# Performance work log

Measured on AMD Instinct MI355X. Metric: run time of the kernel, lower is better.

## Reference

```python
import jax, jax.numpy as jnp
import numpy as np

V, E, CIN, COUT, NH, HID = 8192, 2048, 128, 128, 4, 32
EPS = 1e-5

def _ln(x, g, b):
    m = x.mean(-1, keepdims=True)
    v = x.var(-1, keepdims=True)
    return (x - m) / jnp.sqrt(v + EPS) * g + b

def setup_inputs() -> dict:
    key = jax.random.key(0)
    ks = jax.random.split(key, 12)
    s = 0.05
    X = jax.random.normal(ks[0], (V, CIN), jnp.float32)
    H = jax.random.bernoulli(ks[1], 0.02, (V, E)).astype(jnp.float32)
    edge_features = jax.random.normal(ks[2], (E, COUT), jnp.float32)
    Wv = jax.random.normal(ks[3], (CIN, COUT), jnp.float32) * s
    bv = jnp.zeros((COUT,), jnp.float32)
    We = jax.random.normal(ks[4], (COUT, COUT), jnp.float32) * s
    be = jnp.zeros((COUT,), jnp.float32)
    vW1 = jax.random.normal(ks[5], (NH, CIN, HID), jnp.float32) * s
    vb1 = jnp.zeros((NH, HID), jnp.float32)
    vW2 = jax.random.normal(ks[6], (NH, HID), jnp.float32) * s
    vb2 = jnp.zeros((NH,), jnp.float32)
    eW1 = jax.random.normal(ks[7], (COUT, HID), jnp.float32) * s
    eb1 = jnp.zeros((HID,), jnp.float32)
    eW2 = jax.random.normal(ks[8], (HID,), jnp.float32) * s
    eb2 = jnp.zeros((), jnp.float32)
    Wc = jax.random.normal(ks[9], (NH * COUT, COUT), jnp.float32) * s
    bc = jnp.zeros((COUT,), jnp.float32)
    Wg = jax.random.normal(ks[10], (CIN + COUT, COUT), jnp.float32) * s
    bg = jnp.zeros((COUT,), jnp.float32)
    return dict(X=X, H=H, edge_features=edge_features, Wv=Wv, bv=bv, We=We, be=be,
                vW1=vW1, vb1=vb1, vW2=vW2, vb2=vb2, eW1=eW1, eb1=eb1, eW2=eW2, eb2=eb2,
                Wc=Wc, bc=bc,
                ln_e_g=jnp.ones((COUT,), jnp.float32), ln_e_b=jnp.zeros((COUT,), jnp.float32),
                ln_v_g=jnp.ones((COUT,), jnp.float32), ln_v_b=jnp.zeros((COUT,), jnp.float32),
                bn_g=jnp.ones((COUT,), jnp.float32), bn_b=jnp.zeros((COUT,), jnp.float32),
                Wg=Wg, bg=bg)

def reference(X, H, edge_features, Wv, bv, We, be, vW1, vb1, vW2, vb2,
              eW1, eb1, eW2, eb2, Wc, bc, ln_e_g, ln_e_b, ln_v_g, ln_v_b,
              bn_g, bn_b, Wg, bg):
    gelu = lambda t: jax.nn.gelu(t, approximate=False)  # torch nn.GELU default (erf)
    Ht = H.T                                   # (E, V)
    Xt = X @ Wv + bv                           # (V, Cout) theta_v
    # per-head vertex attention MLP: Linear(Cin,32)->GELU->Linear(32,1), vectorized over heads
    hid = gelu(jnp.einsum('vc,hck->hvk', X, vW1) + vb1[:, None, :])
    attn = jax.nn.sigmoid(jnp.einsum('hvk,hk->hv', hid, vW2) + vb2[:, None])  # (NH, V)
    deg = Ht.sum(axis=1, keepdims=True)        # (E, 1) edge degrees
    denom = jnp.maximum(deg, 1.0)
    # degree-normalized attention-weighted v2e aggregation per head
    head_e = jnp.einsum('ev,hvc->hec', Ht, Xt[None] * attn[:, :, None]) / denom[None]
    e_cat = jnp.transpose(head_e, (1, 0, 2)).reshape(E, NH * COUT)  # concat heads dim=1
    e_feat = e_cat @ Wc + bc                   # attn_combine
    # edge attention uses the LAST head's vertex weights (global-var quirk in torch code)
    edge_att = ((Ht @ attn[-1]) / jnp.maximum(deg[:, 0], 1.0))[:, None]  # (E,1)
    # edge-feature gating with e_attention head 0
    te = edge_features @ We + be               # theta_e
    e_scores = gelu(e_feat @ eW1 + eb1) @ eW2 + eb2
    ew = jax.nn.sigmoid(e_scores)[:, None]
    e_feat = e_feat * ew + te * (1.0 - ew)
    # normalize == 'both': layer_norm_e then batch_norm (training-mode batch stats)
    e_feat = _ln(e_feat, ln_e_g, ln_e_b)
    m = e_feat.mean(axis=0)
    v = e_feat.var(axis=0)
    e_feat = (e_feat - m) / jnp.sqrt(v + EPS) * bn_g + bn_b
    # e2v sum aggregation: H @ e_feat
    v_feat = H @ e_feat                        # (V, Cout)
    gate = jax.nn.sigmoid(jnp.concatenate([X, v_feat], axis=1) @ Wg + bg)
    v_feat = gate * v_feat + (1.0 - gate) * Xt
    v_feat = _ln(v_feat, ln_v_g, ln_v_b)
    v_feat = v_feat + X                        # residual (Cin == Cout)
    v_feat = gelu(v_feat)                      # not is_last: activation; dropout = identity (eval)
    e_feat = gelu(e_feat)
    return v_feat, e_feat, edge_att
```

## Files before the change

kernel.cpp:

```cpp
#include <hip/hip_runtime.h>
#include <hip/hip_bf16.h>
#include <math.h>

#define NV 8192
#define NE 2048
#define CIN 128
#define COUT 128
#define NH 4
#define HID 32
#define EPB 2
#define LCAP 256
#define VCAP 96
#define NWORDS (NE / 64)
#define TWORDS (NV / 64)
#define EPSV 1e-5f

__device__ __forceinline__ float gelu_f(float x) {
    return 0.5f * x * (1.0f + erff(x * 0.70710678118654752f));
}
__device__ __forceinline__ float sigmoid_f(float x) {
    return 1.0f / (1.0f + expf(-x));
}

__global__ __launch_bounds__(256) void k_front(
    const float* __restrict__ X, const float* __restrict__ Wv, const float* __restrict__ bv,
    const float* __restrict__ vW1, const float* __restrict__ vb1,
    const float* __restrict__ vW2, const float* __restrict__ vb2,
    const float* __restrict__ H,
    float* __restrict__ Xt, float* __restrict__ attn4,
    unsigned long long* __restrict__ Hbits, int* __restrict__ vdeg, int* __restrict__ vlist)
{
    __shared__ float Xs[2][8][CIN];
    int t = threadIdx.x;
    if (blockIdx.x < NV / 16) {
        int half = t >> 7, tt = t & 127;
        int v0 = blockIdx.x * 16 + half * 8;
        for (int v = 0; v < 8; ++v) Xs[half][v][tt] = X[(size_t)(v0 + v) * CIN + tt];
        __syncthreads();

        float acc[8];
        float bvc = bv[tt];
#pragma unroll
        for (int v = 0; v < 8; ++v) acc[v] = bvc;
        for (int k = 0; k < CIN; ++k) {
            float w = Wv[k * COUT + tt];
#pragma unroll
            for (int v = 0; v < 8; ++v) acc[v] = fmaf(Xs[half][v][k], w, acc[v]);
        }
        for (int v = 0; v < 8; ++v) Xt[(size_t)(v0 + v) * COUT + tt] = acc[v];

        int h = tt >> 5, j = tt & 31;
        float hb = vb1[h * HID + j];
#pragma unroll
        for (int v = 0; v < 8; ++v) acc[v] = hb;
        for (int k = 0; k < CIN; ++k) {
            float w = vW1[(h * CIN + k) * HID + j];
#pragma unroll
            for (int v = 0; v < 8; ++v) acc[v] = fmaf(Xs[half][v][k], w, acc[v]);
        }
        float w2 = vW2[h * HID + j];
        float b2 = vb2[h];
        for (int v = 0; v < 8; ++v) {
            float val = gelu_f(acc[v]) * w2;
#pragma unroll
            for (int m = 16; m >= 1; m >>= 1) val += __shfl_xor(val, m, 64);
            if (j == 0) attn4[(size_t)(v0 + v) * NH + h] = sigmoid_f(val + b2);
        }
    } else {
        int b = blockIdx.x - NV / 16;
        int w = t >> 6;
        int lane = t & 63;
        int v = b * 4 + w;
        const float4* row4 = (const float4*)(H + (size_t)v * NE);
        int base = 0;
        int* vl = vlist + (size_t)v * VCAP;
#pragma unroll
        for (int it = 0; it < NE / 1024; ++it) {
            int e0 = it * 1024 + lane * 16;
            float4 f0 = row4[it * 256 + lane * 4 + 0];
            float4 f1 = row4[it * 256 + lane * 4 + 1];
            float4 f2 = row4[it * 256 + lane * 4 + 2];
            float4 f3 = row4[it * 256 + lane * 4 + 3];
            unsigned int m16 = 0;
            m16 |= (f0.x != 0.0f ? 1u : 0u) << 0;  m16 |= (f0.y != 0.0f ? 1u : 0u) << 1;
            m16 |= (f0.z != 0.0f ? 1u : 0u) << 2;  m16 |= (f0.w != 0.0f ? 1u : 0u) << 3;
            m16 |= (f1.x != 0.0f ? 1u : 0u) << 4;  m16 |= (f1.y != 0.0f ? 1u : 0u) << 5;
            m16 |= (f1.z != 0.0f ? 1u : 0u) << 6;  m16 |= (f1.w != 0.0f ? 1u : 0u) << 7;
            m16 |= (f2.x != 0.0f ? 1u : 0u) << 8;  m16 |= (f2.y != 0.0f ? 1u : 0u) << 9;
            m16 |= (f2.z != 0.0f ? 1u : 0u) << 10; m16 |= (f2.w != 0.0f ? 1u : 0u) << 11;
            m16 |= (f3.x != 0.0f ? 1u : 0u) << 12; m16 |= (f3.y != 0.0f ? 1u : 0u) << 13;
            m16 |= (f3.z != 0.0f ? 1u : 0u) << 14; m16 |= (f3.w != 0.0f ? 1u : 0u) << 15;

            int cnt = __popc(m16);
            int inc = cnt;
#pragma unroll
            for (int s = 1; s < 64; s <<= 1) {
                int y = __shfl_up(inc, s, 64);
                if (lane >= s) inc += y;
            }
            int tot = __shfl(inc, 63, 64);
            int q = lane & 15;
            unsigned int w0 = __shfl(m16, q * 4 + 0, 64);
            unsigned int w1 = __shfl(m16, q * 4 + 1, 64);
            unsigned int w2 = __shfl(m16, q * 4 + 2, 64);
            unsigned int w3 = __shfl(m16, q * 4 + 3, 64);
            if (lane < 16) {
                unsigned long long word = (unsigned long long)w0
                    | ((unsigned long long)w1 << 16)
                    | ((unsigned long long)w2 << 32)
                    | ((unsigned long long)w3 << 48);
                Hbits[(size_t)v * NWORDS + it * 16 + lane] = word;
            }
            int off = base + inc - cnt;
            unsigned int mm = m16;
            while (mm) {
                int j = __ffs(mm) - 1;
                mm &= mm - 1;
                if (off < VCAP) vl[off] = e0 + j;
                ++off;
            }
            base += tot;
        }
        if (lane == 0) vdeg[v] = base;
    }
}

__global__ __launch_bounds__(256) void k_transpose(
    const unsigned long long* __restrict__ Hbits, unsigned long long* __restrict__ HbitsT)
{
    __shared__ unsigned long long rows[64][NWORDS];
    int t = threadIdx.x;
    int vt = blockIdx.x;
    for (int i = t; i < 64 * NWORDS; i += 256)
        rows[i >> 5][i & 31] = Hbits[(size_t)vt * 64 * NWORDS + i];
    __syncthreads();
    int wv = t >> 6;
    int lane = t & 63;
    const unsigned long long M[6] = {
        0xFFFFFFFF00000000ULL, 0xFFFF0000FFFF0000ULL, 0xFF00FF00FF00FF00ULL,
        0xF0F0F0F0F0F0F0F0ULL, 0xCCCCCCCCCCCCCCCCULL, 0xAAAAAAAAAAAAAAAAULL };
    const int js[6] = {32, 16, 8, 4, 2, 1};
#pragma unroll
    for (int itb = 0; itb < 8; ++itb) {
        int it = wv * 8 + itb;
        unsigned long long x = rows[lane][it];
#pragma unroll
        for (int s = 0; s < 6; ++s) {
            int j = js[s];
            unsigned long long y = __shfl_xor(x, j, 64);
            unsigned long long Ms = M[s];
            if ((lane & j) == 0) x = (x & ~Ms) | ((y << j) & Ms);
            else                 x = (x & Ms) | ((y >> j) & ~Ms);
        }
        HbitsT[(size_t)(it * 64 + lane) * TWORDS + vt] = x;
    }
}

__global__ __launch_bounds__(512) void k_edge(
    const float* __restrict__ Xt, const float* __restrict__ attn4,
    const unsigned long long* __restrict__ HbitsT,
    const float* __restrict__ edge_features,
    const float* __restrict__ Wc, const float* __restrict__ bc,
    const float* __restrict__ We, const float* __restrict__ be,
    const float* __restrict__ eW1, const float* __restrict__ eb1,
    const float* __restrict__ eW2, const float* __restrict__ eb2,
    const float* __restrict__ ln_g, const float* __restrict__ ln_b,
    float* __restrict__ e_ln, float* __restrict__ out_att,
    float* __restrict__ bn_sum, float* __restrict__ bn_sq)
{
    __shared__ int lst[EPB][LCAP];
    __shared__ int wsum[EPB][2];
    __shared__ float sc[4096];
    __shared__ float ecat[EPB][NH * COUT];
    __shared__ float efr_s[EPB][COUT];
    __shared__ float efs[EPB][COUT];
    __shared__ float teL[EPB][COUT];
    __shared__ float ews[EPB];
    __shared__ float asp[EPB][4];
    __shared__ float red[EPB][2][2];

    int t = threadIdx.x;
    int g = t >> 8;
    int tg = t & 255;
    int wv = tg >> 6;
    int lane = t & 63;
    int e = blockIdx.x * EPB + g;

    if (tg < 128) efr_s[g][tg] = edge_features[(size_t)e * COUT + tg];

    if (tg < 128) {
        int gw = tg >> 6;
        unsigned long long wd = HbitsT[(size_t)e * TWORDS + tg];
        int cntT = __popcll(wd);
        int inc = cntT;
#pragma unroll
        for (int s = 1; s < 64; s <<= 1) {
            int y = __shfl_up(inc, s, 64);
            if (lane >= s) inc += y;
        }
        if (lane == 63) wsum[g][gw] = inc;
        __syncthreads();
        int base = (gw ? wsum[g][0] : 0) + inc - cntT;
        int vbase = tg * 64;
        unsigned long long mm = wd;
        while (mm) {
            int i = __ffsll(mm) - 1;
            mm &= mm - 1;
            if (base < LCAP) lst[g][base] = vbase + i;
            ++base;
        }
    } else {
        __syncthreads();
    }
    __syncthreads();

    int n0 = wsum[g][0] + wsum[g][1];
    float inv = 1.0f / fmaxf((float)n0, 1.0f);
    int n = n0 < LCAP ? n0 : LCAP;

    float p00 = 0, p10 = 0, p20 = 0, p30 = 0;
    float p01 = 0, p11 = 0, p21 = 0, p31 = 0;
    float as = 0;
#pragma unroll 2
    for (int i = wv; i < n; i += 4) {
        int v = lst[g][i];
        float x0 = Xt[(size_t)v * COUT + lane];
        float x1 = Xt[(size_t)v * COUT + lane + 64];
        float4 a = *(const float4*)(attn4 + (size_t)v * NH);
        p00 = fmaf(x0, a.x, p00);  p01 = fmaf(x1, a.x, p01);
        p10 = fmaf(x0, a.y, p10);  p11 = fmaf(x1, a.y, p11);
        p20 = fmaf(x0, a.z, p20);  p21 = fmaf(x1, a.z, p21);
        p30 = fmaf(x0, a.w, p30);  p31 = fmaf(x1, a.w, p31);
        as += a.w;
    }
    {
        int bi = g * 2048 + wv * 512;
        sc[bi + 0 * COUT + lane] = p00;  sc[bi + 0 * COUT + lane + 64] = p01;
        sc[bi + 1 * COUT + lane] = p10;  sc[bi + 1 * COUT + lane + 64] = p11;
        sc[bi + 2 * COUT + lane] = p20;  sc[bi + 2 * COUT + lane + 64] = p21;
        sc[bi + 3 * COUT + lane] = p30;  sc[bi + 3 * COUT + lane + 64] = p31;
    }
    if (lane == 0) asp[g][wv] = as;
    __syncthreads();

#pragma unroll
    for (int r = 0; r < 2; ++r) {
        int k = tg + r * 256;
        int bi = g * 2048 + k;
        ecat[g][k] = (sc[bi] + sc[bi + 512] + sc[bi + 1024] + sc[bi + 1536]) * inv;
    }
    if (tg == 0) out_att[e] = (asp[g][0] + asp[g][1] + asp[g][2] + asp[g][3]) * inv;
    __syncthreads();

    {
        int g4 = t >> 7, c = t & 127;
        float accW[EPB] = {0, 0};
        const float* wp = Wc + (size_t)(g4 * 128) * COUT + c;
        for (int k = 0; k < 128; ++k) {
            float w = wp[k * COUT];
#pragma unroll
            for (int ee = 0; ee < EPB; ++ee)
                accW[ee] = fmaf(ecat[ee][g4 * 128 + k], w, accW[ee]);
        }
        float accT[EPB] = {0, 0};
        const float* wt = We + (size_t)(g4 * 32) * COUT + c;
        for (int k = 0; k < 32; ++k) {
            float w = wt[k * COUT];
#pragma unroll
            for (int ee = 0; ee < EPB; ++ee)
                accT[ee] = fmaf(efr_s[ee][g4 * 32 + k], w, accT[ee]);
        }
        __syncthreads();
#pragma unroll
        for (int ee = 0; ee < EPB; ++ee) {
            sc[g4 * 256 + ee * 128 + c] = accW[ee];
            sc[1024 + g4 * 256 + ee * 128 + c] = accT[ee];
        }
    }
    __syncthreads();

    if (t < 256) {
        int ee = t >> 7, c = t & 127;
        efs[ee][c] = sc[0 * 256 + ee * 128 + c] + sc[1 * 256 + ee * 128 + c]
                   + sc[2 * 256 + ee * 128 + c] + sc[3 * 256 + ee * 128 + c] + bc[c];
        teL[ee][c] = sc[1024 + 0 * 256 + ee * 128 + c] + sc[1024 + 1 * 256 + ee * 128 + c]
                   + sc[1024 + 2 * 256 + ee * 128 + c] + sc[1024 + 3 * 256 + ee * 128 + c] + be[c];
    }
    __syncthreads();

    if (t < 64) {
        int ee = t >> 5, j = t & 31;
        float hj = eb1[j];
        for (int k = 0; k < COUT; ++k) hj = fmaf(efs[ee][k], eW1[k * HID + j], hj);
        float val = gelu_f(hj) * eW2[j];
#pragma unroll
        for (int m = 16; m >= 1; m >>= 1) val += __shfl_xor(val, m, 32);
        if ((t & 31) == 0) ews[ee] = sigmoid_f(val + eb2[0]);
    }
    __syncthreads();

    float xb = 0;
    if (tg < 128) {
        int gw = tg >> 6;
        float ew = ews[g];
        xb = efs[g][tg] * ew + teL[g][tg] * (1.0f - ew);
        float s = xb, q = xb * xb;
#pragma unroll
        for (int m = 32; m >= 1; m >>= 1) { s += __shfl_xor(s, m, 64); q += __shfl_xor(q, m, 64); }
        if (lane == 0) { red[g][gw][0] = s; red[g][gw][1] = q; }
    }
    __syncthreads();
    if (tg < 128) {
        float S = red[g][0][0] + red[g][1][0];
        float Q = red[g][0][1] + red[g][1][1];
        float m = S * (1.0f / COUT);
        float var = Q * (1.0f / COUT) - m * m;
        float y = (xb - m) * rsqrtf(var + EPSV) * ln_g[tg] + ln_b[tg];
        e_ln[(size_t)e * COUT + tg] = y;
        sc[g * 128 + tg] = y;
        sc[256 + g * 128 + tg] = y * y;
    }
    __syncthreads();
    if (t < 128) {
        float s = sc[t] + sc[128 + t];
        float q = sc[256 + t] + sc[384 + t];
        atomicAdd(&bn_sum[t], s);
        atomicAdd(&bn_sq[t], q);
    }
}

__global__ __launch_bounds__(256) void k_bnapply(const float* __restrict__ e_ln,
    const float* __restrict__ bn_sum, const float* __restrict__ bn_sq,
    const float* __restrict__ bn_g, const float* __restrict__ bn_b,
    float* __restrict__ out_e)
{
    int idx = blockIdx.x * 256 + threadIdx.x;
    int c = idx & 127;
    float m = bn_sum[c] * (1.0f / NE);
    float var = bn_sq[c] * (1.0f / NE) - m * m;
    float x = e_ln[idx];
    float y = (x - m) * rsqrtf(var + EPSV) * bn_g[c] + bn_b[c];
    out_e[idx] = gelu_f(y);
}

__global__ __launch_bounds__(512) void k_vertex2(
    const float* __restrict__ X, const int* __restrict__ vdeg, const int* __restrict__ vlist,
    const float* __restrict__ e_ln,
    const float* __restrict__ bn_sum, const float* __restrict__ bn_sq,
    const float* __restrict__ bn_g, const float* __restrict__ bn_b,
    const float* __restrict__ Xt,
    const float* __restrict__ Wg, const float* __restrict__ bg,
    const float* __restrict__ ln_g, const float* __restrict__ ln_b,
    float* __restrict__ out_v)
{
    __shared__ float XsF[8 * CIN];
    __shared__ float vfF[8 * COUT];
    __shared__ int lst[8][VCAP];
    __shared__ int degs[8];
    __shared__ float part[4 * 8 * COUT];
    __shared__ float red[8][2][2];

    int t = threadIdx.x;
    int vg = t >> 6, lane = t & 63;
    int g4 = t >> 7, c = t & 127;
    int gw2 = (t >> 6) & 1;
    int v0 = blockIdx.x * 8;

    {
        float2 x2 = *(const float2*)(X + (size_t)(v0 + vg) * CIN + lane * 2);
        XsF[vg * CIN + lane * 2] = x2.x;
        XsF[vg * CIN + lane * 2 + 1] = x2.y;
    }
    for (int i = t; i < 8 * VCAP; i += 512)
        lst[i / VCAP][i % VCAP] = vlist[(size_t)v0 * VCAP + i];
    if (t < 8) degs[t] = vdeg[v0 + t];
    __syncthreads();

    int ch0 = lane * 2;
    float m0 = bn_sum[ch0] * (1.0f / NE);
    float m1 = bn_sum[ch0 + 1] * (1.0f / NE);
    float A0 = bn_g[ch0] * rsqrtf(bn_sq[ch0] * (1.0f / NE) - m0 * m0 + EPSV);
    float A1 = bn_g[ch0 + 1] * rsqrtf(bn_sq[ch0 + 1] * (1.0f / NE) - m1 * m1 + EPSV);
    float B0 = bn_b[ch0] - m0 * A0;
    float B1 = bn_b[ch0 + 1] - m1 * A1;

    int n = degs[vg];
    if (n > VCAP) n = VCAP;
    float sx = 0, sy = 0;
    for (int i = 0; i < n; ++i) {
        float2 v2 = *(const float2*)(e_ln + (size_t)lst[vg][i] * COUT + ch0);
        sx += v2.x;
        sy += v2.y;
    }
    float fn = (float)n;
    vfF[vg * COUT + ch0] = A0 * sx + fn * B0;
    vfF[vg * COUT + ch0 + 1] = A1 * sy + fn * B1;
    __syncthreads();

    {
        float accW[8] = {0, 0, 0, 0, 0, 0, 0, 0};
        const float* wp = Wg + (size_t)(g4 * 64) * COUT + c;
        const float* src = (g4 < 2) ? XsF : vfF;
        int kb = (g4 & 1) * 64;
        for (int ki = 0; ki < 64; ++ki) {
            float w = wp[(size_t)ki * COUT];
#pragma unroll
            for (int v = 0; v < 8; ++v)
                accW[v] = fmaf(src[v * 128 + kb + ki], w, accW[v]);
        }
#pragma unroll
        for (int v = 0; v < 8; ++v) part[g4 * 1024 + v * COUT + c] = accW[v];
    }
    __syncthreads();

    float xv[2];
#pragma unroll
    for (int rep = 0; rep < 2; ++rep) {
        int v = g4 + rep * 4;
        float ag = part[0 * 1024 + v * COUT + c] + part[1 * 1024 + v * COUT + c]
                 + part[2 * 1024 + v * COUT + c] + part[3 * 1024 + v * COUT + c] + bg[c];
        float gate = sigmoid_f(ag);
        float x = gate * vfF[v * COUT + c] + (1.0f - gate) * Xt[(size_t)(v0 + v) * COUT + c];
        xv[rep] = x;
        float s = x, q = x * x;
#pragma unroll
        for (int m = 32; m >= 1; m >>= 1) { s += __shfl_xor(s, m, 64); q += __shfl_xor(q, m, 64); }
        if (lane == 0) { red[v][gw2][0] = s; red[v][gw2][1] = q; }
    }
    __syncthreads();
#pragma unroll
    for (int rep = 0; rep < 2; ++rep) {
        int v = g4 + rep * 4;
        float S = red[v][0][0] + red[v][1][0];
        float Q = red[v][0][1] + red[v][1][1];
        float m_ = S * (1.0f / COUT);
        float var = Q * (1.0f / COUT) - m_ * m_;
        float y = (xv[rep] - m_) * rsqrtf(var + EPSV) * ln_g[c] + ln_b[c];
        y = y + XsF[v * CIN + c];
        out_v[(size_t)(v0 + v) * COUT + c] = gelu_f(y);
    }
}

extern "C" void kernel_launch(void* const* d_in, const int* in_sizes, int n_in,
                              void* d_out, int out_size, void* d_ws, size_t ws_size,
                              hipStream_t stream) {
    const float* X    = (const float*)d_in[0];
    const float* H    = (const float*)d_in[1];
    const float* edge_features = (const float*)d_in[2];
    const float* Wv   = (const float*)d_in[3];
    const float* bv   = (const float*)d_in[4];
    const float* We   = (const float*)d_in[5];
    const float* be   = (const float*)d_in[6];
    const float* vW1  = (const float*)d_in[7];
    const float* vb1  = (const float*)d_in[8];
    const float* vW2  = (const float*)d_in[9];
    const float* vb2  = (const float*)d_in[10];
    const float* eW1  = (const float*)d_in[11];
    const float* eb1  = (const float*)d_in[12];
    const float* eW2  = (const float*)d_in[13];
    const float* eb2  = (const float*)d_in[14];
    const float* Wc   = (const float*)d_in[15];
    const float* bc   = (const float*)d_in[16];
    const float* ln_e_g = (const float*)d_in[17];
    const float* ln_e_b = (const float*)d_in[18];
    const float* ln_v_g = (const float*)d_in[19];
    const float* ln_v_b = (const float*)d_in[20];
    const float* bn_g = (const float*)d_in[21];
    const float* bn_b = (const float*)d_in[22];
    const float* Wg   = (const float*)d_in[23];
    const float* bg   = (const float*)d_in[24];

    float* out_v  = (float*)d_out;
    float* out_e  = out_v + NV * COUT;
    float* out_att = out_e + NE * COUT;

    char* w = (char*)d_ws;
    float* Xt     = (float*)w; w += (size_t)NV * COUT * 4;
    float* attn4  = (float*)w; w += (size_t)NV * NH * 4;
    float* e_ln   = (float*)w; w += (size_t)NE * COUT * 4;
    float* bn_sum = (float*)w; w += COUT * 4;
    float* bn_sq  = (float*)w; w += COUT * 4;
    int*   vdeg   = (int*)w;   w += (size_t)NV * 4;
    int*   vlist  = (int*)w;   w += (size_t)NV * VCAP * 4;
    unsigned long long* Hbits  = (unsigned long long*)w; w += (size_t)NV * NWORDS * 8;
    unsigned long long* HbitsT = (unsigned long long*)w; w += (size_t)NE * TWORDS * 8;

    hipMemsetAsync(bn_sum, 0, 2 * COUT * sizeof(float), stream);

    k_front<<<NV / 16 + NV / 4, 256, 0, stream>>>(X, Wv, bv, vW1, vb1, vW2, vb2, H,
                                                  Xt, attn4, Hbits, vdeg, vlist);
    k_transpose<<<NV / 64, 256, 0, stream>>>(Hbits, HbitsT);
    k_edge<<<NE / EPB, 512, 0, stream>>>(Xt, attn4, HbitsT, edge_features,
                                         Wc, bc, We, be, eW1, eb1, eW2, eb2,
                                         ln_e_g, ln_e_b, e_ln, out_att, bn_sum, bn_sq);
    k_bnapply<<<(NE * COUT) / 256, 256, 0, stream>>>(e_ln, bn_sum, bn_sq, bn_g, bn_b, out_e);
    k_vertex2<<<NV / 8, 512, 0, stream>>>(X, vdeg, vlist, e_ln, bn_sum, bn_sq, bn_g, bn_b,
                                          Xt, Wg, bg, ln_v_g, ln_v_b, out_v);
}
```

Baseline: 268.7 us.

## Split edge kernel into gather-aggregate and tiled dense combine kernels

The fused per-edge kernel is split in two. The first kernel handles one edge per block and does the sparse gather and aggregation, writing the concatenated head features to a global buffer. The second processes 8 edges per block for the Wc/We projections, gating, layer norm and batch-norm partial sums, so each weight load is reused across more edges and fewer atomics are issued. The cost is an extra global round trip for the 4 MB intermediate and one more kernel launch.

```diff
diff --git a/kernel.cpp b/kernel.cpp
--- a/kernel.cpp
+++ b/kernel.cpp
@@ -8,7 +8,7 @@
 #define COUT 128
 #define NH 4
 #define HID 32
-#define EPB 2
+#define ETILE 8
 #define LCAP 256
 #define VCAP 96
 #define NWORDS (NE / 64)
@@ -156,65 +156,45 @@
     }
 }
 
-__global__ __launch_bounds__(512) void k_edge(
+__global__ __launch_bounds__(256) void k_agg(
     const float* __restrict__ Xt, const float* __restrict__ attn4,
     const unsigned long long* __restrict__ HbitsT,
-    const float* __restrict__ edge_features,
-    const float* __restrict__ Wc, const float* __restrict__ bc,
-    const float* __restrict__ We, const float* __restrict__ be,
-    const float* __restrict__ eW1, const float* __restrict__ eb1,
-    const float* __restrict__ eW2, const float* __restrict__ eb2,
-    const float* __restrict__ ln_g, const float* __restrict__ ln_b,
-    float* __restrict__ e_ln, float* __restrict__ out_att,
-    float* __restrict__ bn_sum, float* __restrict__ bn_sq)
-{
-    __shared__ int lst[EPB][LCAP];
-    __shared__ int wsum[EPB][2];
-    __shared__ float sc[4096];
-    __shared__ float ecat[EPB][NH * COUT];
-    __shared__ float efr_s[EPB][COUT];
-    __shared__ float efs[EPB][COUT];
-    __shared__ float teL[EPB][COUT];
-    __shared__ float ews[EPB];
-    __shared__ float asp[EPB][4];
-    __shared__ float red[EPB][2][2];
+    float* __restrict__ ecat_g, float* __restrict__ out_att)
+{
+    __shared__ int lst[LCAP];
+    __shared__ int wsum[2];
+    __shared__ float pt[4][NH][COUT];
+    __shared__ float asp[4];
 
     int t = threadIdx.x;
-    int g = t >> 8;
-    int tg = t & 255;
-    int wv = tg >> 6;
-    int lane = t & 63;
-    int e = blockIdx.x * EPB + g;
-
-    if (tg < 128) efr_s[g][tg] = edge_features[(size_t)e * COUT + tg];
-
-    if (tg < 128) {
-        int gw = tg >> 6;
-        unsigned long long wd = HbitsT[(size_t)e * TWORDS + tg];
-        int cntT = __popcll(wd);
-        int inc = cntT;
-#pragma unroll
-        for (int s = 1; s < 64; s <<= 1) {
-            int y = __shfl_up(inc, s, 64);
-            if (lane >= s) inc += y;
-        }
-        if (lane == 63) wsum[g][gw] = inc;
-        __syncthreads();
-        int base = (gw ? wsum[g][0] : 0) + inc - cntT;
-        int vbase = tg * 64;
+    int wid = t >> 6, lane = t & 63;
+    int e = blockIdx.x;
+
+    unsigned long long wd = 0ull;
+    if (t < 128) wd = HbitsT[(size_t)e * TWORDS + t];
+    int cnt = __popcll(wd);
+    int inc = cnt;
+#pragma unroll
+    for (int s = 1; s < 64; s <<= 1) {
+        int y = __shfl_up(inc, s, 64);
+        if (lane >= s) inc += y;
+    }
+    if (lane == 63 && wid < 2) wsum[wid] = inc;
+    __syncthreads();
+    int n0 = wsum[0] + wsum[1];
+    if (t < 128) {
+        int base = (wid ? wsum[0] : 0) + inc - cnt;
+        int vbase = t * 64;
         unsigned long long mm = wd;
         while (mm) {
             int i = __ffsll(mm) - 1;
             mm &= mm - 1;
-            if (base < LCAP) lst[g][base] = vbase + i;
+            if (base < LCAP) lst[base] = vbase + i;
             ++base;
         }
-    } else {
-        __syncthreads();
-    }
-    __syncthreads();
-
-    int n0 = wsum[g][0] + wsum[g][1];
+    }
+    __syncthreads();
+
     float inv = 1.0f / fmaxf((float)n0, 1.0f);
     int n = n0 < LCAP ? n0 : LCAP;
 
@@ -222,8 +202,8 @@
     float p01 = 0, p11 = 0, p21 = 0, p31 = 0;
     float as = 0;
 #pragma unroll 2
-    for (int i = wv; i < n; i += 4) {
-        int v = lst[g][i];
+    for (int i = wid; i < n; i += 4) {
+        int v = lst[i];
         float x0 = Xt[(size_t)v * COUT + lane];
         float x1 = Xt[(size_t)v * COUT + lane + 64];
         float4 a = *(const float4*)(attn4 + (size_t)v * NH);
@@ -233,97 +213,106 @@
         p30 = fmaf(x0, a.w, p30);  p31 = fmaf(x1, a.w, p31);
         as += a.w;
     }
-    {
-        int bi = g * 2048 + wv * 512;
-        sc[bi + 0 * COUT + lane] = p00;  sc[bi + 0 * COUT + lane + 64] = p01;
-        sc[bi + 1 * COUT + lane] = p10;  sc[bi + 1 * COUT + lane + 64] = p11;
-        sc[bi + 2 * COUT + lane] = p20;  sc[bi + 2 * COUT + lane + 64] = p21;
-        sc[bi + 3 * COUT + lane] = p30;  sc[bi + 3 * COUT + lane + 64] = p31;
-    }
-    if (lane == 0) asp[g][wv] = as;
+    pt[wid][0][lane] = p00;  pt[wid][0][lane + 64] = p01;
+    pt[wid][1][lane] = p10;  pt[wid][1][lane + 64] = p11;
+    pt[wid][2][lane] = p20;  pt[wid][2][lane + 64] = p21;
+    pt[wid][3][lane] = p30;  pt[wid][3][lane + 64] = p31;
+    if (lane == 0) asp[wid] = as;
     __syncthreads();
 
 #pragma unroll
     for (int r = 0; r < 2; ++r) {
-        int k = tg + r * 256;
-        int bi = g * 2048 + k;
-        ecat[g][k] = (sc[bi] + sc[bi + 512] + sc[bi + 1024] + sc[bi + 1536]) * inv;
-    }
-    if (tg == 0) out_att[e] = (asp[g][0] + asp[g][1] + asp[g][2] + asp[g][3]) * inv;
-    __syncthreads();
-
-    {
-        int g4 = t >> 7, c = t & 127;
-        float accW[EPB] = {0, 0};
-        const float* wp = Wc + (size_t)(g4 * 128) * COUT + c;
-        for (int k = 0; k < 128; ++k) {
-            float w = wp[k * COUT];
-#pragma unroll
-            for (int ee = 0; ee < EPB; ++ee)
-                accW[ee] = fmaf(ecat[ee][g4 * 128 + k], w, accW[ee]);
-        }
-        float accT[EPB] = {0, 0};
-        const float* wt = We + (size_t)(g4 * 32) * COUT + c;
-        for (int k = 0; k < 32; ++k) {
-            float w = wt[k * COUT];
-#pragma unroll
-            for (int ee = 0; ee < EPB; ++ee)
-                accT[ee] = fmaf(efr_s[ee][g4 * 32 + k], w, accT[ee]);
-        }
-        __syncthreads();
-#pragma unroll
-        for (int ee = 0; ee < EPB; ++ee) {
-            sc[g4 * 256 + ee * 128 + c] = accW[ee];
-            sc[1024 + g4 * 256 + ee * 128 + c] = accT[ee];
-        }
-    }
-    __syncthreads();
-
-    if (t < 256) {
-        int ee = t >> 7, c = t & 127;
-        efs[ee][c] = sc[0 * 256 + ee * 128 + c] + sc[1 * 256 + ee * 128 + c]
-                   + sc[2 * 256 + ee * 128 + c] + sc[3 * 256 + ee * 128 + c] + bc[c];
-        teL[ee][c] = sc[1024 + 0 * 256 + ee * 128 + c] + sc[1024 + 1 * 256 + ee * 128 + c]
-                   + sc[1024 + 2 * 256 + ee * 128 + c] + sc[1024 + 3 * 256 + ee * 128 + c] + be[c];
-    }
-    __syncthreads();
-
-    if (t < 64) {
+        int k = t + r * 256;
+        int h = k >> 7, ch = k & 127;
+        float s = pt[0][h][ch] + pt[1][h][ch] + pt[2][h][ch] + pt[3][h][ch];
+        ecat_g[(size_t)e * 512 + k] = s * inv;
+    }
+    if (t == 0) out_att[e] = (asp[0] + asp[1] + asp[2] + asp[3]) * inv;
+}
+
+__global__ __launch_bounds__(512) void k_combine(
+    const float* __restrict__ ecat_g, const float* __restrict__ edge_features,
+    const float* __restrict__ Wc, const float* __restrict__ bc,
+    const float* __restrict__ We, const float* __restrict__ be,
+    const float* __restrict__ eW1, const float* __restrict__ eb1,
+    const float* __restrict__ eW2, const float* __restrict__ eb2,
+    const float* __restrict__ ln_g, const float* __restrict__ ln_b,
+    float* __restrict__ e_ln, float* __restrict__ bn_sum, float* __restrict__ bn_sq)
+{
+    __shared__ float ecs[ETILE][512];
+    __shared__ float efr[ETILE][COUT];
+    __shared__ float efs[ETILE][COUT];
+    __shared__ float teL[ETILE][COUT];
+    __shared__ float yb[ETILE][COUT];
+    __shared__ float ews[ETILE];
+    __shared__ float red[ETILE][2][2];
+
+    int t = threadIdx.x;
+    int e0 = blockIdx.x * ETILE;
+    int eslot = t >> 7, c = t & 127;
+    int lane = t & 63;
+    int gw = (t >> 6) & 1;
+
+    for (int idx = t; idx < ETILE * 512; idx += 512)
+        ecs[idx >> 9][idx & 511] = ecat_g[(size_t)e0 * 512 + idx];
+    for (int idx = t; idx < ETILE * COUT; idx += 512)
+        efr[idx >> 7][idx & 127] = edge_features[(size_t)e0 * COUT + idx];
+    __syncthreads();
+
+    float accW0 = 0, accW1 = 0;
+    for (int k = 0; k < 512; ++k) {
+        float w = Wc[(size_t)k * COUT + c];
+        accW0 = fmaf(ecs[eslot][k], w, accW0);
+        accW1 = fmaf(ecs[eslot + 4][k], w, accW1);
+    }
+    float accT0 = 0, accT1 = 0;
+    for (int k = 0; k < COUT; ++k) {
+        float w = We[(size_t)k * COUT + c];
+        accT0 = fmaf(efr[eslot][k], w, accT0);
+        accT1 = fmaf(efr[eslot + 4][k], w, accT1);
+    }
+    float bcc = bc[c], bec = be[c];
+    efs[eslot][c] = accW0 + bcc;
+    efs[eslot + 4][c] = accW1 + bcc;
+    teL[eslot][c] = accT0 + bec;
+    teL[eslot + 4][c] = accT1 + bec;
+    __syncthreads();
+
+    if (t < ETILE * 32) {
         int ee = t >> 5, j = t & 31;
         float hj = eb1[j];
         for (int k = 0; k < COUT; ++k) hj = fmaf(efs[ee][k], eW1[k * HID + j], hj);
         float val = gelu_f(hj) * eW2[j];
 #pragma unroll
         for (int m = 16; m >= 1; m >>= 1) val += __shfl_xor(val, m, 32);
-        if ((t & 31) == 0) ews[ee] = sigmoid_f(val + eb2[0]);
-    }
-    __syncthreads();
-
-    float xb = 0;
-    if (tg < 128) {
-        int gw = tg >> 6;
-        float ew = ews[g];
-        xb = efs[g][tg] * ew + teL[g][tg] * (1.0f - ew);
-        float s = xb, q = xb * xb;
+        if (j == 0) ews[ee] = sigmoid_f(val + eb2[0]);
+    }
+    __syncthreads();
+
+#pragma unroll
+    for (int j = 0; j < 2; ++j) {
+        int e = eslot + 4 * j;
+        float ew = ews[e];
+        float x = efs[e][c] * ew + teL[e][c] * (1.0f - ew);
+        float s = x, q = x * x;
 #pragma unroll
         for (int m = 32; m >= 1; m >>= 1) { s += __shfl_xor(s, m, 64); q += __shfl_xor(q, m, 64); }
-        if (lane == 0) { red[g][gw][0] = s; red[g][gw][1] = q; }
-    }
-    __syncthreads();
-    if (tg < 128) {
-        float S = red[g][0][0] + red[g][1][0];
-        float Q = red[g][0][1] + red[g][1][1];
-        float m = S * (1.0f / COUT);
-        float var = Q * (1.0f / COUT) - m * m;
-        float y = (xb - m) * rsqrtf(var + EPSV) * ln_g[tg] + ln_b[tg];
-        e_ln[(size_t)e * COUT + tg] = y;
-        sc[g * 128 + tg] = y;
-        sc[256 + g * 128 + tg] = y * y;
-    }
-    __syncthreads();
+        if (lane == 0) { red[e][gw][0] = s; red[e][gw][1] = q; }
+        __syncthreads();
+        float S = red[e][0][0] + red[e][1][0];
+        float Q = red[e][0][1] + red[e][1][1];
+        float m_ = S * (1.0f / COUT);
+        float var = Q * (1.0f / COUT) - m_ * m_;
+        float y = (x - m_) * rsqrtf(var + EPSV) * ln_g[c] + ln_b[c];
+        e_ln[(size_t)(e0 + e) * COUT + c] = y;
+        yb[e][c] = y;
+        __syncthreads();
+    }
+
     if (t < 128) {
-        float s = sc[t] + sc[128 + t];
-        float q = sc[256 + t] + sc[384 + t];
+        float s = 0, q = 0;
+#pragma unroll
+        for (int e = 0; e < ETILE; ++e) { float y = yb[e][t]; s += y; q += y * y; }
         atomicAdd(&bn_sum[t], s);
         atomicAdd(&bn_sq[t], q);
     }
@@ -478,6 +467,7 @@
     float* Xt     = (float*)w; w += (size_t)NV * COUT * 4;
     float* attn4  = (float*)w; w += (size_t)NV * NH * 4;
     float* e_ln   = (float*)w; w += (size_t)NE * COUT * 4;
+    float* ecat_g = (float*)w; w += (size_t)NE * NH * COUT * 4;
     float* bn_sum = (float*)w; w += COUT * 4;
     float* bn_sq  = (float*)w; w += COUT * 4;
     int*   vdeg   = (int*)w;   w += (size_t)NV * 4;
@@ -490,9 +480,10 @@
     k_front<<<NV / 16 + NV / 4, 256, 0, stream>>>(X, Wv, bv, vW1, vb1, vW2, vb2, H,
                                                   Xt, attn4, Hbits, vdeg, vlist);
     k_transpose<<<NV / 64, 256, 0, stream>>>(Hbits, HbitsT);
-    k_edge<<<NE / EPB, 512, 0, stream>>>(Xt, attn4, HbitsT, edge_features,
-                                         Wc, bc, We, be, eW1, eb1, eW2, eb2,
-                                         ln_e_g, ln_e_b, e_ln, out_att, bn_sum, bn_sq);
+    k_agg<<<NE, 256, 0, stream>>>(Xt, attn4, HbitsT, ecat_g, out_att);
+    k_combine<<<NE / ETILE, 512, 0, stream>>>(ecat_g, edge_features,
+                                              Wc, bc, We, be, eW1, eb1, eW2, eb2,
+                                              ln_e_g, ln_e_b, e_ln, bn_sum, bn_sq);
     k_bnapply<<<(NE * COUT) / 256, 256, 0, stream>>>(e_ln, bn_sum, bn_sq, bn_g, bn_b, out_e);
     k_vertex2<<<NV / 8, 512, 0, stream>>>(X, vdeg, vlist, e_ln, bn_sum, bn_sq, bn_g, bn_b,
                                           Xt, Wg, bg, ln_v_g, ln_v_b, out_v);
```

Result: no change. 269.5 us (+0.3%).
